# Kernel optimization log

Measured on AMD Instinct MI355X. Metric: run time of the kernel, lower is better.

Reference implementation:

```python
import jax, jax.numpy as jnp
import numpy as np

NUM_CLASSES = 100
FEATURE_DIM = 128
N_SAMPLES = 1_000_000
EPS = 1e-8  # matches F.cosine_similarity eps clamp


def setup_inputs() -> dict:
    key = jax.random.key(0)
    k1, k2 = jax.random.split(key)
    train_feature = jax.random.normal(k1, (N_SAMPLES, FEATURE_DIM), dtype=jnp.float32)
    train_label = jax.random.randint(k2, (N_SAMPLES,), 0, NUM_CLASSES, dtype=jnp.int64)
    return {"train_feature": train_feature, "train_label": train_label}


def reference(train_feature, train_label):
    # Original math per class c with n = |c| samples:
    #   A[i,j] = cos(f_i, f_j) for i != j, then A /= (n-1) (if n > 1)
    #   P_c = (sum_k mean(A[k]) * f_k) / n
    # Key identity: row_sum_k of the cosine matrix (excluding diagonal)
    #   = u_k . (sum_{j in c} u_j) - u_k . u_k, where u = f / max(||f||, eps).
    # So no N x N matrix is ever needed -- pure segment reductions.
    labels = train_label.astype(jnp.int32)
    norms = jnp.linalg.norm(train_feature, axis=1, keepdims=True)
    u = train_feature / jnp.maximum(norms, EPS)  # [N, d] unit vectors

    counts = jax.ops.segment_sum(
        jnp.ones((train_feature.shape[0],), dtype=train_feature.dtype),
        labels, num_segments=NUM_CLASSES)  # [C]
    m = jax.ops.segment_sum(u, labels, num_segments=NUM_CLASSES)  # [C, d]

    n_c = counts[labels]  # [N] class size per sample
    self_sim = jnp.sum(u * u, axis=1)  # == 1 for nonzero rows (0 if f == 0)
    row_sum = jnp.sum(u * m[labels], axis=1) - self_sim  # [N]

    # weight_k = row_mean(A)_k = row_sum / ((n-1) * n); n==1 gives row_sum == 0
    denom = jnp.maximum(n_c - 1.0, 1.0) * jnp.maximum(n_c, 1.0)
    w = row_sum / denom  # [N]

    proto_sum = jax.ops.segment_sum(w[:, None] * train_feature, labels,
                                    num_segments=NUM_CLASSES)  # [C, d]
    prototypes = proto_sum / jnp.maximum(counts, 1.0)[:, None]
    return prototypes
```

## Files before the change

kernel.cpp:

```cpp
#include <hip/hip_runtime.h>


namespace {

constexpr int C = 100;
constexpr int D = 128;
constexpr float EPS = 1e-8f;
constexpr int BLOCK = 256;
constexpr int GRID = 768;

__global__ __launch_bounds__(BLOCK) void k_stats(const float* __restrict__ feat,
                                                 const int* __restrict__ lab,
                                                 float* __restrict__ m_g,
                                                 float* __restrict__ cnt_g,
                                                 int n) {
  __shared__ float m_loc[C * D];
  __shared__ float cnt_loc[C];
  for (int i = threadIdx.x; i < C * D; i += BLOCK) m_loc[i] = 0.f;
  if (threadIdx.x < C) cnt_loc[threadIdx.x] = 0.f;
  __syncthreads();

  const int lane = threadIdx.x & 63;
  const int wid = (blockIdx.x * BLOCK + threadIdx.x) >> 6;
  const int nw = (GRID * BLOCK) >> 6;

  for (int i = wid; i < n; i += nw) {
    const float* row = feat + (size_t)i * D;
    float x0 = row[lane];
    float x1 = row[lane + 64];
    float ss = x0 * x0 + x1 * x1;
#pragma unroll
    for (int off = 32; off > 0; off >>= 1) ss += __shfl_xor(ss, off, 64);
    float inv = 1.0f / fmaxf(sqrtf(ss), EPS);
    int c = lab[i];
    atomicAdd(&m_loc[c * D + lane], x0 * inv);
    atomicAdd(&m_loc[c * D + lane + 64], x1 * inv);
    if (lane == 0) atomicAdd(&cnt_loc[c], 1.0f);
  }
  __syncthreads();

  for (int i = threadIdx.x; i < C * D; i += BLOCK) atomicAdd(&m_g[i], m_loc[i]);
  if (threadIdx.x < C) atomicAdd(&cnt_g[threadIdx.x], cnt_loc[threadIdx.x]);
}

__global__ __launch_bounds__(BLOCK) void k_proto(const float* __restrict__ feat,
                                                 const int* __restrict__ lab,
                                                 const float* __restrict__ m_g,
                                                 const float* __restrict__ cnt_g,
                                                 float* __restrict__ proto_g,
                                                 int n) {
  __shared__ float p_loc[C * D];
  __shared__ float cnt_loc[C];
  for (int i = threadIdx.x; i < C * D; i += BLOCK) p_loc[i] = 0.f;
  if (threadIdx.x < C) cnt_loc[threadIdx.x] = cnt_g[threadIdx.x];
  __syncthreads();

  const int lane = threadIdx.x & 63;
  const int wid = (blockIdx.x * BLOCK + threadIdx.x) >> 6;
  const int nw = (GRID * BLOCK) >> 6;

  for (int i = wid; i < n; i += nw) {
    const float* row = feat + (size_t)i * D;
    int c = lab[i];
    float x0 = row[lane];
    float x1 = row[lane + 64];
    float m0 = m_g[c * D + lane];
    float m1 = m_g[c * D + lane + 64];
    float ss = x0 * x0 + x1 * x1;
    float pm = x0 * m0 + x1 * m1;
#pragma unroll
    for (int off = 32; off > 0; off >>= 1) {
      ss += __shfl_xor(ss, off, 64);
      pm += __shfl_xor(pm, off, 64);
    }
    float inv = 1.0f / fmaxf(sqrtf(ss), EPS);
    float row_sum = pm * inv - ss * inv * inv;
    float nc = cnt_loc[c];
    float w = row_sum / (fmaxf(nc - 1.f, 1.f) * fmaxf(nc, 1.f));
    atomicAdd(&p_loc[c * D + lane], w * x0);
    atomicAdd(&p_loc[c * D + lane + 64], w * x1);
  }
  __syncthreads();

  for (int i = threadIdx.x; i < C * D; i += BLOCK) atomicAdd(&proto_g[i], p_loc[i]);
}

__global__ void k_final(const float* __restrict__ proto_g,
                        const float* __restrict__ cnt_g,
                        float* __restrict__ out) {
  int i = blockIdx.x * BLOCK + threadIdx.x;
  if (i < C * D) out[i] = proto_g[i] / fmaxf(cnt_g[i / D], 1.f);
}

}

extern "C" void kernel_launch(void* const* d_in, const int* in_sizes, int n_in,
                              void* d_out, int out_size, void* d_ws, size_t ws_size,
                              hipStream_t stream) {
  const float* feat = (const float*)d_in[0];
  const int* lab = (const int*)d_in[1];
  const int n = in_sizes[0] / D;

  float* m_g = (float*)d_ws;
  float* cnt_g = m_g + C * D;
  float* proto_g = cnt_g + C;
  hipMemsetAsync(d_ws, 0, (size_t)(2 * C * D + C) * sizeof(float), stream);

  k_stats<<<GRID, BLOCK, 0, stream>>>(feat, lab, m_g, cnt_g, n);
  k_proto<<<GRID, BLOCK, 0, stream>>>(feat, lab, m_g, cnt_g, proto_g, n);
  k_final<<<(C * D + BLOCK - 1) / BLOCK, BLOCK, 0, stream>>>(proto_g, cnt_g, (float*)d_out);
}
```

Before: 2.073 ms.

## Vectorize row loads with float4 and process eight rows per wavefront iteration

Each wavefront now handles two rows at once, one per 32-lane half, loading features as float4. It loops over four such pairs per iteration to raise memory-level parallelism and batch the shuffle reductions. The shared-memory accumulator uses a permuted layout, component-major within each class row, so the four atomics per lane stay bank-friendly, and the final flush to global memory undoes the permutation. The risks are more register pressure and tail handling through clamped indices plus validity flags.

Result: faster. 1.914 ms (-7.7%).

```diff
diff --git a/kernel.cpp b/kernel.cpp
--- a/kernel.cpp
+++ b/kernel.cpp
@@ -8,8 +8,9 @@
 constexpr float EPS = 1e-8f;
 constexpr int BLOCK = 256;
 constexpr int GRID = 768;
+constexpr int S = 8;
 
-__global__ __launch_bounds__(BLOCK) void k_stats(const float* __restrict__ feat,
+__global__ __launch_bounds__(BLOCK) void k_stats(const float4* __restrict__ feat4,
                                                  const int* __restrict__ lab,
                                                  float* __restrict__ m_g,
                                                  float* __restrict__ cnt_g,
@@ -21,31 +22,56 @@
   __syncthreads();
 
   const int lane = threadIdx.x & 63;
+  const int half = lane >> 5;
+  const int sl = lane & 31;
   const int wid = (blockIdx.x * BLOCK + threadIdx.x) >> 6;
   const int nw = (GRID * BLOCK) >> 6;
 
-  for (int i = wid; i < n; i += nw) {
-    const float* row = feat + (size_t)i * D;
-    float x0 = row[lane];
-    float x1 = row[lane + 64];
-    float ss = x0 * x0 + x1 * x1;
+  for (int base = wid * S; base < n; base += nw * S) {
+    float4 x[4];
+    int c[4];
+    bool valid[4];
 #pragma unroll
-    for (int off = 32; off > 0; off >>= 1) ss += __shfl_xor(ss, off, 64);
-    float inv = 1.0f / fmaxf(sqrtf(ss), EPS);
-    int c = lab[i];
-    atomicAdd(&m_loc[c * D + lane], x0 * inv);
-    atomicAdd(&m_loc[c * D + lane + 64], x1 * inv);
-    if (lane == 0) atomicAdd(&cnt_loc[c], 1.0f);
+    for (int s = 0; s < 4; ++s) {
+      int idx = base + 2 * s + half;
+      valid[s] = idx < n;
+      int ci = valid[s] ? idx : n - 1;
+      x[s] = feat4[(size_t)ci * 32 + sl];
+      c[s] = lab[ci];
+    }
+    float ss[4];
+#pragma unroll
+    for (int s = 0; s < 4; ++s)
+      ss[s] = x[s].x * x[s].x + x[s].y * x[s].y + x[s].z * x[s].z + x[s].w * x[s].w;
+#pragma unroll
+    for (int off = 16; off > 0; off >>= 1) {
+#pragma unroll
+      for (int s = 0; s < 4; ++s) ss[s] += __shfl_xor(ss[s], off, 64);
+    }
+#pragma unroll
+    for (int s = 0; s < 4; ++s) {
+      if (!valid[s]) continue;
+      float inv = 1.0f / fmaxf(sqrtf(ss[s]), EPS);
+      float* mp = &m_loc[c[s] * D];
+      atomicAdd(&mp[0 * 32 + sl], x[s].x * inv);
+      atomicAdd(&mp[1 * 32 + sl], x[s].y * inv);
+      atomicAdd(&mp[2 * 32 + sl], x[s].z * inv);
+      atomicAdd(&mp[3 * 32 + sl], x[s].w * inv);
+      if (sl == 0) atomicAdd(&cnt_loc[c[s]], 1.0f);
+    }
   }
   __syncthreads();
 
-  for (int i = threadIdx.x; i < C * D; i += BLOCK) atomicAdd(&m_g[i], m_loc[i]);
+  for (int i = threadIdx.x; i < C * D; i += BLOCK) {
+    int cls = i >> 7, a = i & 127, q = a >> 5, s2 = a & 31;
+    atomicAdd(&m_g[cls * D + s2 * 4 + q], m_loc[i]);
+  }
   if (threadIdx.x < C) atomicAdd(&cnt_g[threadIdx.x], cnt_loc[threadIdx.x]);
 }
 
-__global__ __launch_bounds__(BLOCK) void k_proto(const float* __restrict__ feat,
+__global__ __launch_bounds__(BLOCK) void k_proto(const float4* __restrict__ feat4,
                                                  const int* __restrict__ lab,
-                                                 const float* __restrict__ m_g,
+                                                 const float4* __restrict__ m_g4,
                                                  const float* __restrict__ cnt_g,
                                                  float* __restrict__ proto_g,
                                                  int n) {
@@ -56,33 +82,60 @@
   __syncthreads();
 
   const int lane = threadIdx.x & 63;
+  const int half = lane >> 5;
+  const int sl = lane & 31;
   const int wid = (blockIdx.x * BLOCK + threadIdx.x) >> 6;
   const int nw = (GRID * BLOCK) >> 6;
 
-  for (int i = wid; i < n; i += nw) {
-    const float* row = feat + (size_t)i * D;
-    int c = lab[i];
-    float x0 = row[lane];
-    float x1 = row[lane + 64];
-    float m0 = m_g[c * D + lane];
-    float m1 = m_g[c * D + lane + 64];
-    float ss = x0 * x0 + x1 * x1;
-    float pm = x0 * m0 + x1 * m1;
+  for (int base = wid * S; base < n; base += nw * S) {
+    float4 x[4], mv[4];
+    int c[4];
+    bool valid[4];
 #pragma unroll
-    for (int off = 32; off > 0; off >>= 1) {
-      ss += __shfl_xor(ss, off, 64);
-      pm += __shfl_xor(pm, off, 64);
+    for (int s = 0; s < 4; ++s) {
+      int idx = base + 2 * s + half;
+      valid[s] = idx < n;
+      int ci = valid[s] ? idx : n - 1;
+      x[s] = feat4[(size_t)ci * 32 + sl];
+      c[s] = lab[ci];
     }
-    float inv = 1.0f / fmaxf(sqrtf(ss), EPS);
-    float row_sum = pm * inv - ss * inv * inv;
-    float nc = cnt_loc[c];
-    float w = row_sum / (fmaxf(nc - 1.f, 1.f) * fmaxf(nc, 1.f));
-    atomicAdd(&p_loc[c * D + lane], w * x0);
-    atomicAdd(&p_loc[c * D + lane + 64], w * x1);
+#pragma unroll
+    for (int s = 0; s < 4; ++s) mv[s] = m_g4[c[s] * 32 + sl];
+
+    float ss[4], pm[4];
+#pragma unroll
+    for (int s = 0; s < 4; ++s) {
+      ss[s] = x[s].x * x[s].x + x[s].y * x[s].y + x[s].z * x[s].z + x[s].w * x[s].w;
+      pm[s] = x[s].x * mv[s].x + x[s].y * mv[s].y + x[s].z * mv[s].z + x[s].w * mv[s].w;
+    }
+#pragma unroll
+    for (int off = 16; off > 0; off >>= 1) {
+#pragma unroll
+      for (int s = 0; s < 4; ++s) {
+        ss[s] += __shfl_xor(ss[s], off, 64);
+        pm[s] += __shfl_xor(pm[s], off, 64);
+      }
+    }
+#pragma unroll
+    for (int s = 0; s < 4; ++s) {
+      if (!valid[s]) continue;
+      float inv = 1.0f / fmaxf(sqrtf(ss[s]), EPS);
+      float row_sum = pm[s] * inv - ss[s] * inv * inv;
+      float nc = cnt_loc[c[s]];
+      float w = row_sum / (fmaxf(nc - 1.f, 1.f) * fmaxf(nc, 1.f));
+      float* pp = &p_loc[c[s] * D];
+      atomicAdd(&pp[0 * 32 + sl], w * x[s].x);
+      atomicAdd(&pp[1 * 32 + sl], w * x[s].y);
+      atomicAdd(&pp[2 * 32 + sl], w * x[s].z);
+      atomicAdd(&pp[3 * 32 + sl], w * x[s].w);
+    }
   }
   __syncthreads();
 
-  for (int i = threadIdx.x; i < C * D; i += BLOCK) atomicAdd(&proto_g[i], p_loc[i]);
+  for (int i = threadIdx.x; i < C * D; i += BLOCK) {
+    int cls = i >> 7, a = i & 127, q = a >> 5, s2 = a & 31;
+    atomicAdd(&proto_g[cls * D + s2 * 4 + q], p_loc[i]);
+  }
 }
 
 __global__ void k_final(const float* __restrict__ proto_g,
@@ -106,7 +159,8 @@
   float* proto_g = cnt_g + C;
   hipMemsetAsync(d_ws, 0, (size_t)(2 * C * D + C) * sizeof(float), stream);
 
-  k_stats<<<GRID, BLOCK, 0, stream>>>(feat, lab, m_g, cnt_g, n);
-  k_proto<<<GRID, BLOCK, 0, stream>>>(feat, lab, m_g, cnt_g, proto_g, n);
+  k_stats<<<GRID, BLOCK, 0, stream>>>((const float4*)feat, lab, m_g, cnt_g, n);
+  k_proto<<<GRID, BLOCK, 0, stream>>>((const float4*)feat, lab, (const float4*)m_g,
+                                      cnt_g, proto_g, n);
   k_final<<<(C * D + BLOCK - 1) / BLOCK, BLOCK, 0, stream>>>(proto_g, cnt_g, (float*)d_out);
 }
```
